# Performance work log

Measured on AMD Instinct MI355X. Metric: run time of the kernel, lower is better.

Reference implementation:

```python
import jax, jax.numpy as jnp
import numpy as np

D_MODEL = 1024
N_HEAD = 16
DIM_PER_HEAD = D_MODEL // N_HEAD
B, S = 8, 1024


def setup_inputs() -> dict:
    key = jax.random.key(0)
    ks = jax.random.split(key, 12)
    s = 0.02
    return {
        "k": jax.random.normal(ks[0], (B, S, D_MODEL), jnp.float32),
        "v": jax.random.normal(ks[1], (B, S, D_MODEL), jnp.float32),
        "q": jax.random.normal(ks[2], (B, S, D_MODEL), jnp.float32),
        "attn_mask": jax.random.randint(ks[3], (B, S, S), 0, 2, jnp.int32),
        "Wk": jax.random.normal(ks[4], (D_MODEL, D_MODEL), jnp.float32) * s,
        "bk": jnp.zeros((D_MODEL,), jnp.float32),
        "Wv": jax.random.normal(ks[5], (D_MODEL, D_MODEL), jnp.float32) * s,
        "bv": jnp.zeros((D_MODEL,), jnp.float32),
        "Wq": jax.random.normal(ks[6], (D_MODEL, D_MODEL), jnp.float32) * s,
        "bq": jnp.zeros((D_MODEL,), jnp.float32),
        "Wo": jax.random.normal(ks[7], (D_MODEL, D_MODEL), jnp.float32) * s,
        "bo": jnp.zeros((D_MODEL,), jnp.float32),
    }


def reference(k, v, q, attn_mask, Wk, bk, Wv, bv, Wq, bq, Wo, bo):
    batch, key_len, _ = k.shape
    query_len = q.shape[1]
    scale = 1.0 / jnp.sqrt(jnp.float32(DIM_PER_HEAD))

    def split_heads(x):  # [b, s, d] -> [b, h, s, dh]
        return x.reshape(batch, -1, N_HEAD, DIM_PER_HEAD).transpose(0, 2, 1, 3)

    key_up = split_heads(k @ Wk + bk)
    value_up = split_heads(v @ Wv + bv)
    query_up = split_heads(q @ Wq + bq) * scale

    # [b, h, q, k] scores; mask nonzero entries with -inf (masked_fill_ semantics)
    scores = jnp.einsum("bhqd,bhkd->bhqk", query_up, key_up)
    scores = jnp.where(attn_mask[:, None, :, :] != 0, -jnp.inf, scores)
    attn = jax.nn.softmax(scores, axis=-1)
    # NOTE: original applies dropout but discards the result; attn (pre-dropout) is used.
    context = jnp.einsum("bhqk,bhkd->bhqd", attn, value_up)
    context = context.transpose(0, 2, 1, 3).reshape(batch, query_len, D_MODEL)
    output = context @ Wo + bo
    attn_mean = attn.sum(axis=1) / N_HEAD  # [b, q, k]
    return output, attn_mean
```

## Files before the change

### kernel.cpp

```cpp
#include <hip/hip_runtime.h>
#include <hip/hip_bf16.h>

typedef unsigned short u16;
typedef unsigned int u32;
typedef __attribute__((ext_vector_type(8))) short bf16x8;
typedef __attribute__((ext_vector_type(4))) float f32x4;
typedef __attribute__((ext_vector_type(4))) u16 u16x4;
typedef __attribute__((ext_vector_type(4))) u32 u32x4;

#define DEV static __device__ __forceinline__

DEV u16 f2bf(float x) {
  unsigned u = __builtin_bit_cast(unsigned, x);
  u += 0x7fffu + ((u >> 16) & 1u);
  return (u16)(u >> 16);
}
DEV float bf2f(u16 u) { return __builtin_bit_cast(float, ((unsigned)u) << 16); }

DEV u32 cvtpk(float lo, float hi) {
  u32 r;
  asm("v_cvt_pk_bf16_f32 %0, %1, %2" : "=v"(r) : "v"(lo), "v"(hi));
  return r;
}

DEV void glds16(const u16* g, u16* l) {
  __builtin_amdgcn_global_load_lds(
      (const __attribute__((address_space(1))) void*)g,
      (__attribute__((address_space(3))) void*)l, 16, 0, 0);
}

__global__ __launch_bounds__(256) void xcvt(
    const float* __restrict__ k, const float* __restrict__ v,
    const float* __restrict__ q, u16* __restrict__ Xb) {
  const size_t i0 = (size_t)blockIdx.x * 256 + threadIdx.x;
  for (size_t t = i0; t < 6291456; t += 524288) {
    const size_t e = t * 4;
    const float* src = (e < 8388608) ? k + e
                     : (e < 16777216) ? v + (e - 8388608)
                     : q + (e - 16777216);
    const f32x4 x = *(const f32x4*)src;
    u16x4 o;
#pragma unroll
    for (int r = 0; r < 4; ++r) o[r] = f2bf(x[r]);
    *(u16x4*)&Xb[e] = o;
  }
}

__global__ __launch_bounds__(256) void transpose_w(
    const float* __restrict__ w0, const float* __restrict__ w1,
    const float* __restrict__ w2, const float* __restrict__ w3,
    u16* __restrict__ out) {
  __shared__ u16 tile[32][33];
  const int mat = blockIdx.y;
  const float* in = (mat == 0) ? w0 : (mat == 1) ? w1 : (mat == 2) ? w2 : w3;
  u16* o = out + (size_t)mat * 1048576;
  const int bk = ((int)blockIdx.x & 31) << 5;
  const int bn = ((int)blockIdx.x >> 5) << 5;
  const int tx = threadIdx.x & 31, ty = threadIdx.x >> 5;
#pragma unroll
  for (int i = 0; i < 32; i += 8)
    tile[ty + i][tx] = f2bf(in[(size_t)(bk + ty + i) * 1024 + bn + tx]);
  __syncthreads();
#pragma unroll
  for (int i = 0; i < 32; i += 8)
    o[(size_t)(bn + ty + i) * 1024 + bk + tx] = tile[tx][ty + i];
}

__global__ __launch_bounds__(256) void maskpack(
    const int* __restrict__ mask, unsigned long long* __restrict__ Mb) {
  const int qt = blockIdx.x, b = blockIdx.y;
  const int tid = threadIdx.x;
  const int w = tid >> 6, l = tid & 63;
  const int ln = l & 15, lg = l >> 4;
  const int* Mp = mask + ((size_t)b << 20) + ((size_t)(qt << 4) << 10);
  unsigned long long m = 0ull;
#pragma unroll
  for (int t = 0; t < 16; ++t) {
    const int key = (w << 8) + (t << 4) + ln;
#pragma unroll
    for (int r = 0; r < 4; ++r) {
      const int row = (lg << 2) + r;
      if (Mp[((size_t)row << 10) + key] != 0) m |= 1ull << ((t << 2) + r);
    }
  }
  Mb[((((size_t)b << 6) + qt) << 8) + tid] = m;
}

__global__ __launch_bounds__(256) void gemm_qkv(
    const u16* __restrict__ Xb, const u16* __restrict__ WTall,
    const float* __restrict__ bK, const float* __restrict__ bV,
    const float* __restrict__ bQ,
    u16* __restrict__ Kup, u16* __restrict__ VupT, u16* __restrict__ Qup) {
  __shared__ u16 As[4096];
  __shared__ u16 Bs[4096];
  const int mode = blockIdx.y;
  const u16* A = Xb + (size_t)mode * 8388608;
  const u16* Bw = WTall + (size_t)mode * 1048576;
  const float* bias = (mode == 0) ? bK : (mode == 1) ? bV : bQ;

  const int tid = threadIdx.x;
  const int w = tid >> 6, l = tid & 63;
  const int ln = l & 15, lg = l >> 4, kg8 = lg << 3;
  const int wr = w >> 1, wc = w & 1;
  const int mb = ((int)blockIdx.x >> 3) << 7;
  const int nb = ((int)blockIdx.x & 7) << 7;

  const int srow = (w << 5) + (l >> 2);
  const int sseg = (l & 3) << 3;
  const u16* Ag0 = A + (size_t)(mb + srow) * 1024 + sseg;
  const u16* Bg0 = Bw + (size_t)(nb + srow) * 1024 + sseg;
  u16* Al0 = As + srow * 32 + sseg;
  u16* Bl0 = Bs + srow * 32 + sseg;

  f32x4 acc[4][4] = {};
  const int ar = (wr << 6) + ln;
  const int br = (wc << 6) + ln;

  for (int k0 = 0; k0 < 1024; k0 += 32) {
    glds16(Ag0 + k0, Al0);
    glds16(Ag0 + 16384 + k0, Al0 + 512);
    glds16(Bg0 + k0, Bl0);
    glds16(Bg0 + 16384 + k0, Bl0 + 512);
    __syncthreads();
    bf16x8 aa[4], bb[4];
#pragma unroll
    for (int mt = 0; mt < 4; ++mt) aa[mt] = *(const bf16x8*)&As[(ar + (mt << 4)) * 32 + kg8];
#pragma unroll
    for (int nt = 0; nt < 4; ++nt) bb[nt] = *(const bf16x8*)&Bs[(br + (nt << 4)) * 32 + kg8];
#pragma unroll
    for (int mt = 0; mt < 4; ++mt)
#pragma unroll
      for (int nt = 0; nt < 4; ++nt)
        acc[mt][nt] = __builtin_amdgcn_mfma_f32_16x16x32_bf16(aa[mt], bb[nt], acc[mt][nt], 0, 0, 0);
    __syncthreads();
  }

  const float scale = (mode == 2) ? 0.125f : 1.0f;
#pragma unroll
  for (int mt = 0; mt < 4; ++mt) {
    const int m0 = mb + (wr << 6) + (mt << 4) + (lg << 2);
    const int bb_ = m0 >> 10, s0 = m0 & 1023;
#pragma unroll
    for (int nt = 0; nt < 4; ++nt) {
      const int n = nb + (wc << 6) + (nt << 4) + ln;
      const float bval = bias[n];
      const int h = n >> 6, dh = n & 63;
      const size_t bh = (size_t)(bb_ * 16 + h);
      if (mode == 1) {
        const int wv = dh >> 4, lnv = dh & 15;
        const int kk = s0 >> 5, lgv = (s0 >> 3) & 3, e0 = s0 & 7;
        u16x4 pk;
#pragma unroll
        for (int r = 0; r < 4; ++r) pk[r] = f2bf(acc[mt][nt][r] + bval);
        *(u16x4*)&VupT[(bh << 16) + (wv << 14) + (kk << 9) + (lgv << 7) +
                       (lnv << 3) + e0] = pk;
      } else if (mode == 0) {
        const int half = dh >> 5, lg2 = (dh >> 3) & 3, e = dh & 7;
        const int T = s0 >> 4;
        u16* base = Kup + (bh << 16) + (T << 10) + (half << 9) + (lg2 << 7) + e;
#pragma unroll
        for (int r = 0; r < 4; ++r)
          base[((s0 & 15) + r) << 3] = f2bf(acc[mt][nt][r] + bval);
      } else {
#pragma unroll
        for (int r = 0; r < 4; ++r)
          Qup[((bh << 10) + s0 + r) * 64 + dh] =
              f2bf((acc[mt][nt][r] + bval) * scale);
      }
    }
  }
}

__global__ __launch_bounds__(256) void gemm_out(
    const u16* __restrict__ Ctx, const u16* __restrict__ WTall,
    const float* __restrict__ bO, float* __restrict__ Out) {
  __shared__ u16 As[4096];
  __shared__ u16 Bs[4096];
  const u16* Bw = WTall + 3145728;

  const int tid = threadIdx.x;
  const int w = tid >> 6, l = tid & 63;
  const int ln = l & 15, lg = l >> 4, kg8 = lg << 3;
  const int wr = w >> 1, wc = w & 1;
  const int mb = ((int)blockIdx.x >> 3) << 7;
  const int nb = ((int)blockIdx.x & 7) << 7;

  const int srow = (w << 5) + (l >> 2);
  const int sseg = (l & 3) << 3;
  const u16* Ag0 = Ctx + (size_t)(mb + srow) * 1024 + sseg;
  const u16* Bg0 = Bw + (size_t)(nb + srow) * 1024 + sseg;
  u16* Al0 = As + srow * 32 + sseg;
  u16* Bl0 = Bs + srow * 32 + sseg;

  f32x4 acc[4][4] = {};
  const int ar = (wr << 6) + ln;
  const int br = (wc << 6) + ln;

  for (int k0 = 0; k0 < 1024; k0 += 32) {
    glds16(Ag0 + k0, Al0);
    glds16(Ag0 + 16384 + k0, Al0 + 512);
    glds16(Bg0 + k0, Bl0);
    glds16(Bg0 + 16384 + k0, Bl0 + 512);
    __syncthreads();
    bf16x8 aa[4], bb[4];
#pragma unroll
    for (int mt = 0; mt < 4; ++mt) aa[mt] = *(const bf16x8*)&As[(ar + (mt << 4)) * 32 + kg8];
#pragma unroll
    for (int nt = 0; nt < 4; ++nt) bb[nt] = *(const bf16x8*)&Bs[(br + (nt << 4)) * 32 + kg8];
#pragma unroll
    for (int mt = 0; mt < 4; ++mt)
#pragma unroll
      for (int nt = 0; nt < 4; ++nt)
        acc[mt][nt] = __builtin_amdgcn_mfma_f32_16x16x32_bf16(aa[mt], bb[nt], acc[mt][nt], 0, 0, 0);
    __syncthreads();
  }
#pragma unroll
  for (int mt = 0; mt < 4; ++mt) {
    const int m0 = mb + (wr << 6) + (mt << 4) + (lg << 2);
#pragma unroll
    for (int nt = 0; nt < 4; ++nt) {
      const int n = nb + (wc << 6) + (nt << 4) + ln;
      const float bval = bO[n];
#pragma unroll
      for (int r = 0; r < 4; ++r)
        Out[(size_t)(m0 + r) * 1024 + n] = acc[mt][nt][r] + bval;
    }
  }
}

__global__ __launch_bounds__(256, 2) void attn_kernel(
    const u16* __restrict__ Qup, const u16* __restrict__ Kf,
    const u16* __restrict__ Vf, const unsigned long long* __restrict__ Mb,
    u16* __restrict__ Ctx, u16* __restrict__ Pp) {
  __shared__ u16 P_lds[16 * 1024];
  __shared__ float red_s[4][16];
  __shared__ float invs[16];

  const int tid = threadIdx.x;
  const int w = tid >> 6, l = tid & 63;
  const int ln = l & 15, lg = l >> 4;
  const int kg8 = lg << 3;

  const int bid = (int)blockIdx.x;
  const int swz = ((bid & 7) << 9) | (bid >> 3);
  const int qt = swz & 63;
  const int qb = qt << 4;
  const int b = (swz >> 6) & 7;
  const int hs = swz >> 9;

  const unsigned long long mbits = Mb[((((size_t)b << 6) + qt) << 8) + tid];

  u32x4 accp[8];

#pragma unroll 1
  for (int hh = 0; hh < 2; ++hh) {
    const int h = (hs << 1) + hh;
    const size_t bh = (size_t)(b * 16 + h);
    const u16* Qp = Qup + ((bh << 10) + qb) * 64;
    const u16* Kb = Kf + (bh << 16);
    const u16* Vb = Vf + (bh << 16) + ((size_t)w << 14);

    const bf16x8 qa0 = *(const bf16x8*)&Qp[ln * 64 + kg8];
    const bf16x8 qa1 = *(const bf16x8*)&Qp[ln * 64 + 32 + kg8];

    bf16x8 ka[3], kb[3];
#pragma unroll
    for (int p = 0; p < 3; ++p) {
      const int To = ((w << 4) + p) << 10;
      ka[p] = *(const bf16x8*)&Kb[To + (l << 3)];
      kb[p] = *(const bf16x8*)&Kb[To + 512 + (l << 3)];
    }

    float rsum[4] = {0, 0, 0, 0};
#pragma unroll
    for (int t = 0; t < 16; ++t) {
      const int s = t % 3;
      const bf16x8 k0 = ka[s], k1 = kb[s];
      if (t + 3 < 16) {
        const int To = ((w << 4) + t + 3) << 10;
        ka[s] = *(const bf16x8*)&Kb[To + (l << 3)];
        kb[s] = *(const bf16x8*)&Kb[To + 512 + (l << 3)];
      }
      f32x4 c = {0, 0, 0, 0};
      c = __builtin_amdgcn_mfma_f32_16x16x32_bf16(qa0, k0, c, 0, 0, 0);
      c = __builtin_amdgcn_mfma_f32_16x16x32_bf16(qa1, k1, c, 0, 0, 0);
      const int key = (w << 8) + (t << 4) + ln;
      float p[4];
#pragma unroll
      for (int r = 0; r < 4; ++r) {
        p[r] = ((mbits >> ((t << 2) + r)) & 1ull) ? 0.0f : __expf(c[r] - 4.0f);
        rsum[r] += p[r];
      }
      const u32 pk01 = cvtpk(p[0], p[1]);
      const u32 pk23 = cvtpk(p[2], p[3]);
      const int r0 = lg << 2;
      *(u16*)((char*)P_lds + ((((r0 + 0) << 11) + (key << 1)) ^ (((r0 + 0) & 7) << 4))) = (u16)pk01;
      *(u16*)((char*)P_lds + ((((r0 + 1) << 11) + (key << 1)) ^ (((r0 + 1) & 7) << 4))) = (u16)(pk01 >> 16);
      *(u16*)((char*)P_lds + ((((r0 + 2) << 11) + (key << 1)) ^ (((r0 + 2) & 7) << 4))) = (u16)pk23;
      *(u16*)((char*)P_lds + ((((r0 + 3) << 11) + (key << 1)) ^ (((r0 + 3) & 7) << 4))) = (u16)(pk23 >> 16);
    }
#pragma unroll
    for (int off = 1; off < 16; off <<= 1) {
#pragma unroll
      for (int r = 0; r < 4; ++r) rsum[r] += __shfl_xor(rsum[r], off);
    }
    if (ln == 0) {
#pragma unroll
      for (int r = 0; r < 4; ++r) red_s[w][(lg << 2) + r] = rsum[r];
    }

    bf16x8 vr[4];
#pragma unroll
    for (int p = 0; p < 4; ++p)
      vr[p] = *(const bf16x8*)&Vb[(p << 9) + (l << 3)];

    __syncthreads();
    float inv[4];
#pragma unroll
    for (int r = 0; r < 4; ++r) {
      const int row = (lg << 2) + r;
      inv[r] = 1.0f / (red_s[0][row] + red_s[1][row] + red_s[2][row] + red_s[3][row]);
    }
    if (ln == 0) {
#pragma unroll
      for (int r = 0; r < 4; ++r) invs[(lg << 2) + r] = inv[r];
    }

    f32x4 c0 = {0, 0, 0, 0}, c1 = {0, 0, 0, 0};
#pragma unroll
    for (int kk = 0; kk < 32; ++kk) {
      const int s = kk & 3;
      const bf16x8 vb = vr[s];
      if (kk + 4 < 32)
        vr[s] = *(const bf16x8*)&Vb[((kk + 4) << 9) + (l << 3)];
      const int a0 = ((ln << 11) + (((kk << 5) + kg8) << 1)) ^ ((ln & 7) << 4);
      const bf16x8 pa = *(const bf16x8*)((const char*)P_lds + a0);
      if (kk & 1)
        c1 = __builtin_amdgcn_mfma_f32_16x16x32_bf16(pa, vb, c1, 0, 0, 0);
      else
        c0 = __builtin_amdgcn_mfma_f32_16x16x32_bf16(pa, vb, c0, 0, 0, 0);
    }
    {
      const u32 q01 = cvtpk((c0[0] + c1[0]) * inv[0], (c0[1] + c1[1]) * inv[1]);
      const u32 q23 = cvtpk((c0[2] + c1[2]) * inv[2], (c0[3] + c1[3]) * inv[3]);
      u16* Cp = &Ctx[(((size_t)b << 10) + qb + (lg << 2)) * 1024 + (h << 6) + (w << 4) + ln];
      Cp[0] = (u16)q01;
      Cp[1024] = (u16)(q01 >> 16);
      Cp[2048] = (u16)q23;
      Cp[3072] = (u16)(q23 >> 16);
    }

    {
      const int row = tid >> 4;
      const float iv = invs[row];
      u16* Pg = Pp + ((size_t)hs << 23) + (((size_t)b << 10) + qb + row) * 1024;
#pragma unroll
      for (int i = 0; i < 8; ++i) {
        const int chunk = (tid & 15) + (i << 4);
        const int bo_ = ((row << 11) + (chunk << 4)) ^ ((row & 7) << 4);
        const u32x4 pu = *(const u32x4*)((const char*)P_lds + bo_);
        u32x4 o;
#pragma unroll
        for (int j = 0; j < 4; ++j) {
          const float plo = __builtin_bit_cast(float, pu[j] << 16) * iv;
          const float phi = __builtin_bit_cast(float, pu[j] & 0xFFFF0000u) * iv;
          if (hh == 0) {
            o[j] = cvtpk(plo, phi);
          } else {
            const u32 a = accp[i][j];
            const float alo = __builtin_bit_cast(float, a << 16);
            const float ahi = __builtin_bit_cast(float, a & 0xFFFF0000u);
            o[j] = cvtpk(alo + plo, ahi + phi);
          }
        }
        if (hh == 0) accp[i] = o;
        else *(u32x4*)&Pg[chunk << 3] = o;
      }
    }
    __syncthreads();
  }
}

__global__ __launch_bounds__(256) void combine(
    const u16* __restrict__ Pp, float* __restrict__ Am) {
  const size_t i = ((size_t)blockIdx.x * 256 + threadIdx.x) * 8;
  float s[8] = {0, 0, 0, 0, 0, 0, 0, 0};
#pragma unroll
  for (int p = 0; p < 8; ++p) {
    const u16x4* q = (const u16x4*)&Pp[(size_t)p * 8388608 + i];
    const u16x4 a = q[0], c = q[1];
#pragma unroll
    for (int r = 0; r < 4; ++r) { s[r] += bf2f(a[r]); s[r + 4] += bf2f(c[r]); }
  }
  f32x4 lo, hi;
#pragma unroll
  for (int r = 0; r < 4; ++r) { lo[r] = s[r] * 0.0625f; hi[r] = s[r + 4] * 0.0625f; }
  *(f32x4*)&Am[i] = lo;
  *(f32x4*)&Am[i + 4] = hi;
}

extern "C" void kernel_launch(void* const* d_in, const int* in_sizes, int n_in,
                              void* d_out, int out_size, void* d_ws, size_t ws_size,
                              hipStream_t stream) {
  const float* k_in = (const float*)d_in[0];
  const float* v_in = (const float*)d_in[1];
  const float* q_in = (const float*)d_in[2];
  const int* mask = (const int*)d_in[3];
  const float* Wk = (const float*)d_in[4];
  const float* bk = (const float*)d_in[5];
  const float* Wv = (const float*)d_in[6];
  const float* bv = (const float*)d_in[7];
  const float* Wq = (const float*)d_in[8];
  const float* bq = (const float*)d_in[9];
  const float* Wo = (const float*)d_in[10];
  const float* bo = (const float*)d_in[11];

  float* out = (float*)d_out;
  float* amean = out + (size_t)8 * 1024 * 1024;

  unsigned long long* Mb = (unsigned long long*)amean;

  u16* ws = (u16*)d_ws;
  u16* WT = ws;
  u16* Xb = ws + 4194304;
  u16* Pp = ws + 4194304;
  u16* Kf   = ws + 71303168;
  u16* Vf   = ws + 79691776;
  u16* Qup  = ws + 88080384;
  u16* Ctx  = ws + 96468992;

  xcvt<<<2048, 256, 0, stream>>>(k_in, v_in, q_in, Xb);
  transpose_w<<<dim3(1024, 4), dim3(256), 0, stream>>>(Wk, Wv, Wq, Wo, WT);
  maskpack<<<dim3(64, 8), dim3(256), 0, stream>>>(mask, Mb);
  gemm_qkv<<<dim3(512, 3), dim3(256), 0, stream>>>(
      Xb, WT, bk, bv, bq, Kf, Vf, Qup);
  attn_kernel<<<dim3(4096), dim3(256), 0, stream>>>(
      Qup, Kf, Vf, Mb, Ctx, Pp);
  combine<<<4096, 256, 0, stream>>>(Pp, amean);
  gemm_out<<<512, 256, 0, stream>>>(Ctx, WT, bo, out);
}
```

Before: 311.9 us.

## Loop all 16 heads per block and write attention mean directly

```diff
diff --git a/kernel.cpp b/kernel.cpp
--- a/kernel.cpp
+++ b/kernel.cpp
@@ -231,7 +231,7 @@
 __global__ __launch_bounds__(256, 2) void attn_kernel(
     const u16* __restrict__ Qup, const u16* __restrict__ Kf,
     const u16* __restrict__ Vf, const unsigned long long* __restrict__ Mb,
-    u16* __restrict__ Ctx, u16* __restrict__ Pp) {
+    u16* __restrict__ Ctx, float* __restrict__ Am) {
   __shared__ u16 P_lds[16 * 1024];
   __shared__ float red_s[4][16];
   __shared__ float invs[16];
@@ -242,20 +242,17 @@
   const int kg8 = lg << 3;
 
   const int bid = (int)blockIdx.x;
-  const int swz = ((bid & 7) << 9) | (bid >> 3);
-  const int qt = swz & 63;
+  const int b = bid & 7;
+  const int qt = bid >> 3;
   const int qb = qt << 4;
-  const int b = (swz >> 6) & 7;
-  const int hs = swz >> 9;
 
   const unsigned long long mbits = Mb[((((size_t)b << 6) + qt) << 8) + tid];
 
   u32x4 accp[8];
 
 #pragma unroll 1
-  for (int hh = 0; hh < 2; ++hh) {
-    const int h = (hs << 1) + hh;
-    const size_t bh = (size_t)(b * 16 + h);
+  for (int hh = 0; hh < 16; ++hh) {
+    const size_t bh = (size_t)(b * 16 + hh);
     const u16* Qp = Qup + ((bh << 10) + qb) * 64;
     const u16* Kb = Kf + (bh << 16);
     const u16* Vb = Vf + (bh << 16) + ((size_t)w << 14);
@@ -343,7 +340,7 @@
     {
       const u32 q01 = cvtpk((c0[0] + c1[0]) * inv[0], (c0[1] + c1[1]) * inv[1]);
       const u32 q23 = cvtpk((c0[2] + c1[2]) * inv[2], (c0[3] + c1[3]) * inv[3]);
-      u16* Cp = &Ctx[(((size_t)b << 10) + qb + (lg << 2)) * 1024 + (h << 6) + (w << 4) + ln];
+      u16* Cp = &Ctx[(((size_t)b << 10) + qb + (lg << 2)) * 1024 + (hh << 6) + (w << 4) + ln];
       Cp[0] = (u16)q01;
       Cp[1024] = (u16)(q01 >> 16);
       Cp[2048] = (u16)q23;
@@ -353,7 +350,6 @@
     {
       const int row = tid >> 4;
       const float iv = invs[row];
-      u16* Pg = Pp + ((size_t)hs << 23) + (((size_t)b << 10) + qb + row) * 1024;
 #pragma unroll
       for (int i = 0; i < 8; ++i) {
         const int chunk = (tid & 15) + (i << 4);
@@ -373,30 +369,30 @@
             o[j] = cvtpk(alo + plo, ahi + phi);
           }
         }
-        if (hh == 0) accp[i] = o;
-        else *(u32x4*)&Pg[chunk << 3] = o;
+        accp[i] = o;
       }
     }
     __syncthreads();
   }
-}
-
-__global__ __launch_bounds__(256) void combine(
-    const u16* __restrict__ Pp, float* __restrict__ Am) {
-  const size_t i = ((size_t)blockIdx.x * 256 + threadIdx.x) * 8;
-  float s[8] = {0, 0, 0, 0, 0, 0, 0, 0};
-#pragma unroll
-  for (int p = 0; p < 8; ++p) {
-    const u16x4* q = (const u16x4*)&Pp[(size_t)p * 8388608 + i];
-    const u16x4 a = q[0], c = q[1];
-#pragma unroll
-    for (int r = 0; r < 4; ++r) { s[r] += bf2f(a[r]); s[r + 4] += bf2f(c[r]); }
-  }
-  f32x4 lo, hi;
-#pragma unroll
-  for (int r = 0; r < 4; ++r) { lo[r] = s[r] * 0.0625f; hi[r] = s[r + 4] * 0.0625f; }
-  *(f32x4*)&Am[i] = lo;
-  *(f32x4*)&Am[i + 4] = hi;
+
+  {
+    const int row = tid >> 4;
+    float* Ag = Am + (((size_t)b << 10) + qb + row) * 1024;
+#pragma unroll
+    for (int i = 0; i < 8; ++i) {
+      const int chunk = (tid & 15) + (i << 4);
+      f32x4 o0, o1;
+#pragma unroll
+      for (int j = 0; j < 4; ++j) {
+        const float lo = __builtin_bit_cast(float, accp[i][j] << 16) * 0.0625f;
+        const float hi = __builtin_bit_cast(float, accp[i][j] & 0xFFFF0000u) * 0.0625f;
+        if (j < 2) { o0[2 * j] = lo; o0[2 * j + 1] = hi; }
+        else       { o1[2 * (j - 2)] = lo; o1[2 * (j - 2) + 1] = hi; }
+      }
+      *(f32x4*)&Ag[chunk << 3] = o0;
+      *(f32x4*)&Ag[(chunk << 3) + 4] = o1;
+    }
+  }
 }
 
 extern "C" void kernel_launch(void* const* d_in, const int* in_sizes, int n_in,
@@ -418,12 +414,10 @@
   float* out = (float*)d_out;
   float* amean = out + (size_t)8 * 1024 * 1024;
 
-  unsigned long long* Mb = (unsigned long long*)amean;
-
   u16* ws = (u16*)d_ws;
   u16* WT = ws;
   u16* Xb = ws + 4194304;
-  u16* Pp = ws + 4194304;
+  unsigned long long* Mb = (unsigned long long*)(ws + 29360128);
   u16* Kf   = ws + 71303168;
   u16* Vf   = ws + 79691776;
   u16* Qup  = ws + 88080384;
@@ -434,8 +428,7 @@
   maskpack<<<dim3(64, 8), dim3(256), 0, stream>>>(mask, Mb);
   gemm_qkv<<<dim3(512, 3), dim3(256), 0, stream>>>(
       Xb, WT, bk, bv, bq, Kf, Vf, Qup);
-  attn_kernel<<<dim3(4096), dim3(256), 0, stream>>>(
-      Qup, Kf, Vf, Mb, Ctx, Pp);
-  combine<<<4096, 256, 0, stream>>>(Pp, amean);
+  attn_kernel<<<dim3(512), dim3(256), 0, stream>>>(
+      Qup, Kf, Vf, Mb, Ctx, amean);
   gemm_out<<<512, 256, 0, stream>>>(Ctx, WT, bo, out);
 }
```

Result: faster. 297.1 us (-4.7%).
